# Optimization experiments

Hardware: AMD Instinct MI355X
Metric: run time of the kernel (lower is better)

The kernel has to match this reference:

```python
import jax, jax.numpy as jnp
import numpy as np

D_IN, H1, H2, B, K = 128, 128, 64, 262144, 4

def _mk(key, shape):
    return jax.random.normal(key, shape, dtype=jnp.float32) * 0.05

def setup_inputs() -> dict:
    key = jax.random.key(0)
    ks = jax.random.split(key, 40)
    inp = {
        'x': jax.random.normal(ks[0], (B, 96), dtype=jnp.float32),
        'u': jax.random.normal(ks[1], (B, 32), dtype=jnp.float32),
        'mix_factor': jax.random.uniform(ks[2], (1,), dtype=jnp.float32),
        'teacher_P': jax.random.uniform(ks[3], (K,), dtype=jnp.float32),
    }
    # main critic params (torch Linear: W [out,in], b [out])
    dims = [(H1, D_IN), (H1, H1), (H2, H1), (1, H2)] * 2  # l1..l4, l5..l8
    for i, (o, ii) in enumerate(dims):
        inp[f'W{i+1}'] = _mk(ks[4 + 2 * i], (o, ii))
        inp[f'b{i+1}'] = _mk(ks[5 + 2 * i], (o,))
    # stacked teacher params (K teachers), only l1,l2,l3,l5,l6,l7 are used
    tdims = {'1': (H1, D_IN), '2': (H1, H1), '3': (H2, H1), '5': (H1, D_IN), '6': (H1, H1), '7': (H2, H1)}
    j = 20
    for name, (o, ii) in tdims.items():
        inp[f'tW{name}'] = _mk(ks[j], (K, o, ii)); j += 1
        inp[f'tb{name}'] = _mk(ks[j], (K, o)); j += 1
    return inp

def reference(x, u, mix_factor, teacher_P, W1, b1, W2, b2, W3, b3, W4, b4, W5, b5, W6, b6, W7, b7, W8, b8, tW1, tb1, tW2, tb2, tW3, tb3, tW5, tb5, tW6, tb6, tW7, tb7):
    m = mix_factor  # [1], broadcasts
    P = teacher_P   # [K]
    xu = jnp.concatenate([x, u], axis=1)  # [B, 128]

    lin = lambda h, W, b: h @ W.T + b
    # teacher linear on shared input [B,I] -> [K,B,O]
    tlin0 = lambda h, W, b: jnp.einsum('bi,koi->kbo', h, W) + b[:, None, :]
    # teacher linear on per-teacher streams [K,B,I] -> [K,B,O]
    tlin = lambda h, W, b: jnp.einsum('kbi,koi->kbo', h, W) + b[:, None, :]
    mixsum = lambda ht: jnp.einsum('kbo,k->bo', ht, P)

    def head(W_a, b_a, W_b, b_b, W_c, b_c, W_d, b_d, tWa, tba, tWb, tbb, tWc, tbc):
        ht = tlin0(xu, tWa, tba)                                   # [K,B,128]
        h = jax.nn.relu(lin(xu, W_a, b_a) * (1 - m) + mixsum(ht) * m)
        ht = jax.nn.relu(ht)
        ht2 = tlin(ht, tWb, tbb)
        h = jax.nn.relu(lin(h, W_b, b_b) * (1 - m) + mixsum(ht2) * m)
        ht2 = jax.nn.relu(ht2)
        ht3 = tlin(ht2, tWc, tbc)
        h = jax.nn.relu(lin(h, W_c, b_c) * (1 - m) + mixsum(ht3) * m)
        return lin(h, W_d, b_d)                                    # [B,1]

    x1 = head(W1, b1, W2, b2, W3, b3, W4, b4, tW1, tb1, tW2, tb2, tW3, tb3)
    x2 = head(W5, b5, W6, b6, W7, b7, W8, b8, tW5, tb5, tW6, tb6, tW7, tb7)
    return (x1, x2)
```

## Files before the change

kernel.cpp:

```cpp
#include <hip/hip_runtime.h>
#include <hip/hip_bf16.h>
#include <stdint.h>

#define B_TOTAL 262144
#define TB 64
#define SLOT 16384
#define BUF1 81920
#define LDS_BYTES 163840
#define HEAD_W 204800

typedef short v8s __attribute__((ext_vector_type(8)));
typedef float v4f __attribute__((ext_vector_type(4)));

union Frag { uint4 q; uint32_t d[4]; v8s v; };

__device__ __forceinline__ unsigned short f2bf(float f) {
    uint32_t u = __float_as_uint(f);
    return (unsigned short)((u + 0x7FFFu + ((u >> 16) & 1u)) >> 16);
}
__device__ __forceinline__ uint32_t pack2(float a, float b) {
    union { __hip_bfloat162 h; uint32_t u; } p;
    p.h = __float22bfloat162_rn(make_float2(a, b));
    return p.u;
}


struct KParams {
    const float* x; const float* u; const float* mix; const float* P;
    const float* mb[6];
    const float* tb[6];
    const float* Wout[2];
    const float* bout[2];
    const unsigned short* wbf;
    float* out;
};

struct PrepParams { const float* src[12]; unsigned short* dst; };

__global__ __launch_bounds__(256) void prep_kernel(PrepParams pp) {
    const int ends[12] = {16384,81920,98304,163840,172032,204800,
                          221184,286720,303104,368640,376832,409600};
    int gi = (blockIdx.x * 256 + threadIdx.x) * 4;
    if (gi >= 409600) return;
    int s = 0;
    #pragma unroll
    for (int i = 0; i < 12; ++i) { if (gi >= ends[i]) s = i + 1; }
    int base = (s == 0) ? 0 : ends[s - 1];
    const float4 f = *(const float4*)(pp.src[s] + (gi - base));
    *(uint2*)(pp.dst + gi) = make_uint2(pack2(f.x, f.y), pack2(f.z, f.w));
}

__device__ __forceinline__ void stage_xu(char* lds, const float* x, const float* u,
                                         int rowBase, int tid)
{
    for (int G = tid; G < 1024; G += 256) {
        const int row = G >> 4;
        const int gg  = G & 15;
        const int grow = rowBase + row;
        float4 fa, fb;
        if (gg < 12) {
            const float* s2 = x + grow * 96 + gg * 8;
            fa = *(const float4*)s2; fb = *(const float4*)(s2 + 4);
        } else {
            const float* s2 = u + grow * 32 + (gg - 12) * 8;
            fa = *(const float4*)s2; fb = *(const float4*)(s2 + 4);
        }
        *(uint4*)(lds + row * 256 + ((gg ^ (row & 15)) << 4)) =
            make_uint4(pack2(fa.x, fa.y), pack2(fa.z, fa.w),
                       pack2(fb.x, fb.y), pack2(fb.z, fb.w));
    }
}

template<bool SHARED_IN, int N>
__device__ __forceinline__ void layer_fwd(char* lds, int inOff, int outOff,
        const unsigned short* W, const float* mbias, const float* tbias,
        float c0, const float* cP, int lane, int wave,
        const float* Wout, float* pgrid)
{
    constexpr int OT = N / 64;
    constexpr bool FINAL = (N == 64);
    const int l15  = lane & 15;
    const int quad = lane >> 4;
    const int cg   = wave;

    v4f acc[5][OT][4];
    #pragma unroll
    for (int s = 0; s < 5; ++s)
        #pragma unroll
        for (int ot = 0; ot < OT; ++ot)
            #pragma unroll
            for (int bt = 0; bt < 4; ++bt)
                acc[s][ot][bt] = (v4f){0.f, 0.f, 0.f, 0.f};

    #pragma unroll
    for (int ks = 0; ks < 4; ++ks) {
        Frag xS[4];
        if constexpr (SHARED_IN) {
            #pragma unroll
            for (int bt = 0; bt < 4; ++bt) {
                const int row = bt * 16 + l15;
                const int gg  = ks * 4 + quad;
                xS[bt].q = *(const uint4*)(lds + inOff + row * 256 + ((gg ^ (row & 15)) << 4));
            }
        }
        #pragma unroll
        for (int s = 0; s < 5; ++s) {
            Frag xF[4];
            if constexpr (!SHARED_IN) {
                #pragma unroll
                for (int bt = 0; bt < 4; ++bt) {
                    const int row = bt * 16 + l15;
                    const int gg  = ks * 4 + quad;
                    xF[bt].q = *(const uint4*)(lds + inOff + s * SLOT + row * 256
                                               + ((gg ^ (row & 15)) << 4));
                }
            }
            Frag wF[OT];
            #pragma unroll
            for (int ot = 0; ot < OT; ++ot) {
                const int o = cg * (OT * 16) + ot * 16 + l15;
                wF[ot].q = *(const uint4*)(W + s * (N * 128) + o * 128 + ks * 32 + quad * 8);
            }
            #pragma unroll
            for (int ot = 0; ot < OT; ++ot)
                #pragma unroll
                for (int bt = 0; bt < 4; ++bt)
                    acc[s][ot][bt] = __builtin_amdgcn_mfma_f32_16x16x32_bf16(
                        wF[ot].v, (SHARED_IN ? xS[bt].v : xF[bt].v), acc[s][ot][bt], 0, 0, 0);
        }
    }

    if constexpr (!FINAL) {
        #pragma unroll
        for (int ot = 0; ot < OT; ++ot) {
            const int obase = cg * 32 + ot * 16 + quad * 4;
            const float4 mB = *(const float4*)(mbias + obase);
            float4 tB[4];
            #pragma unroll
            for (int s = 0; s < 4; ++s)
                tB[s] = *(const float4*)(tbias + s * N + obase);
            #pragma unroll
            for (int bt = 0; bt < 4; ++bt) {
                const int row = bt * 16 + l15;
                char* ab = lds + outOff + row * 256 + (((obase >> 3) ^ (row & 15)) << 4)
                           + ((obase & 7) << 1);
                float vr[4];
                vr[0] = c0 * (acc[0][ot][bt][0] + mB.x);
                vr[1] = c0 * (acc[0][ot][bt][1] + mB.y);
                vr[2] = c0 * (acc[0][ot][bt][2] + mB.z);
                vr[3] = c0 * (acc[0][ot][bt][3] + mB.w);
                uint2 tw[4];
                #pragma unroll
                for (int s = 0; s < 4; ++s) {
                    float t0 = acc[s + 1][ot][bt][0] + tB[s].x;
                    float t1 = acc[s + 1][ot][bt][1] + tB[s].y;
                    float t2 = acc[s + 1][ot][bt][2] + tB[s].z;
                    float t3 = acc[s + 1][ot][bt][3] + tB[s].w;
                    vr[0] = fmaf(cP[s], t0, vr[0]);
                    vr[1] = fmaf(cP[s], t1, vr[1]);
                    vr[2] = fmaf(cP[s], t2, vr[2]);
                    vr[3] = fmaf(cP[s], t3, vr[3]);
                    tw[s] = make_uint2(pack2(fmaxf(t0, 0.f), fmaxf(t1, 0.f)),
                                       pack2(fmaxf(t2, 0.f), fmaxf(t3, 0.f)));
                }
                *(uint2*)ab = make_uint2(pack2(fmaxf(vr[0], 0.f), fmaxf(vr[1], 0.f)),
                                         pack2(fmaxf(vr[2], 0.f), fmaxf(vr[3], 0.f)));
                #pragma unroll
                for (int s = 0; s < 4; ++s)
                    *(uint2*)(ab + (s + 1) * SLOT) = tw[s];
            }
        }
    } else {
        const int obase = cg * 16 + quad * 4;
        const float4 mB = *(const float4*)(mbias + obase);
        float4 tB[4];
        #pragma unroll
        for (int s = 0; s < 4; ++s)
            tB[s] = *(const float4*)(tbias + s * N + obase);
        const float4 wo = *(const float4*)(Wout + obase);
        float psum[4];
        #pragma unroll
        for (int bt = 0; bt < 4; ++bt) {
            float vr[4];
            vr[0] = c0 * (acc[0][0][bt][0] + mB.x);
            vr[1] = c0 * (acc[0][0][bt][1] + mB.y);
            vr[2] = c0 * (acc[0][0][bt][2] + mB.z);
            vr[3] = c0 * (acc[0][0][bt][3] + mB.w);
            #pragma unroll
            for (int s = 0; s < 4; ++s) {
                vr[0] = fmaf(cP[s], acc[s + 1][0][bt][0] + tB[s].x, vr[0]);
                vr[1] = fmaf(cP[s], acc[s + 1][0][bt][1] + tB[s].y, vr[1]);
                vr[2] = fmaf(cP[s], acc[s + 1][0][bt][2] + tB[s].z, vr[2]);
                vr[3] = fmaf(cP[s], acc[s + 1][0][bt][3] + tB[s].w, vr[3]);
            }
            float pp = fmaxf(vr[0], 0.f) * wo.x + fmaxf(vr[1], 0.f) * wo.y
                     + fmaxf(vr[2], 0.f) * wo.z + fmaxf(vr[3], 0.f) * wo.w;
            pp += __shfl_xor(pp, 16);
            pp += __shfl_xor(pp, 32);
            psum[bt] = pp;
        }
        if (lane < 16) {
            #pragma unroll
            for (int bt = 0; bt < 4; ++bt)
                pgrid[cg * 64 + bt * 16 + lane] = psum[bt];
        }
    }
}

extern "C" __global__ __launch_bounds__(256, 1)
void critic_kernel(KParams p)
{
    extern __shared__ char lds[];
    const int tid  = threadIdx.x;
    const int lane = tid & 63;
    const int wave = tid >> 6;
    const int rowBase = blockIdx.x * TB;

    const float m  = p.mix[0];
    const float c0 = 1.f - m;
    float cP[4];
    #pragma unroll
    for (int k = 0; k < 4; ++k) cP[k] = m * p.P[k];

    stage_xu(lds, p.x, p.u, rowBase, tid);

    #pragma unroll 1
    for (int head = 0; head < 2; ++head) {
        __syncthreads();
        const unsigned short* wb = p.wbf + head * HEAD_W;
        const int hb = head * 3;

        layer_fwd<true, 128>(lds, 0, BUF1, wb, p.mb[hb + 0], p.tb[hb + 0],
                             c0, cP, lane, wave, nullptr, nullptr);
        __syncthreads();
        layer_fwd<false, 128>(lds, BUF1, 0, wb + 81920, p.mb[hb + 1], p.tb[hb + 1],
                              c0, cP, lane, wave, nullptr, nullptr);
        __syncthreads();
        layer_fwd<false, 64>(lds, 0, 0, wb + 163840, p.mb[hb + 2], p.tb[hb + 2],
                             c0, cP, lane, wave, p.Wout[head], (float*)(lds + BUF1));
        __syncthreads();

        if (tid < 64) {
            const float* pg = (const float*)(lds + BUF1);
            p.out[head * B_TOTAL + rowBase + tid] =
                p.bout[head][0] + pg[tid] + pg[64 + tid] + pg[128 + tid] + pg[192 + tid];
        }
        if (head == 0)
            stage_xu(lds, p.x, p.u, rowBase, tid);
    }
}

extern "C" void kernel_launch(void* const* d_in, const int* in_sizes, int n_in,
                              void* d_out, int out_size, void* d_ws, size_t ws_size,
                              hipStream_t stream)
{
    (void)in_sizes; (void)n_in; (void)out_size; (void)ws_size;

    PrepParams pp;
    const int sidx[12] = {4, 20, 6, 22, 8, 24, 12, 26, 14, 28, 16, 30};
    for (int i = 0; i < 12; ++i) pp.src[i] = (const float*)d_in[sidx[i]];
    pp.dst = (unsigned short*)d_ws;

    KParams kp;
    kp.x = (const float*)d_in[0];  kp.u = (const float*)d_in[1];
    kp.mix = (const float*)d_in[2]; kp.P = (const float*)d_in[3];
    const int mbi[6] = {5, 7, 9, 13, 15, 17};
    const int tbi[6] = {21, 23, 25, 27, 29, 31};
    for (int i = 0; i < 6; ++i) {
        kp.mb[i] = (const float*)d_in[mbi[i]];
        kp.tb[i] = (const float*)d_in[tbi[i]];
    }
    kp.Wout[0] = (const float*)d_in[10]; kp.Wout[1] = (const float*)d_in[18];
    kp.bout[0] = (const float*)d_in[11]; kp.bout[1] = (const float*)d_in[19];
    kp.wbf = (const unsigned short*)d_ws;
    kp.out = (float*)d_out;

    (void)hipFuncSetAttribute((const void*)critic_kernel,
                              hipFuncAttributeMaxDynamicSharedMemorySize, LDS_BYTES);

    hipLaunchKernelGGL(prep_kernel, dim3(400), dim3(256), 0, stream, pp);
    hipLaunchKernelGGL(critic_kernel, dim3(4096), dim3(256), LDS_BYTES, stream, kp);
}
```

Before: 882.2 us.

## Split layer work across eight waves with 16-column tiles per wave

The critic kernel goes from 256 to 512 threads per block. Each wave now computes one 16-column output tile instead of two, and the final 64-wide layer is split across wave pairs by batch tile. Launch bounds become (512,2) and the input staging loop stride is updated to match. The goal is more waves per CU to hide MFMA and LDS latency. In exchange, each activation fragment is reused across only one weight tile, so LDS reads double, and registers per thread are capped more tightly.

```diff
diff --git a/kernel.cpp b/kernel.cpp
--- a/kernel.cpp
+++ b/kernel.cpp
@@ -14,10 +14,6 @@
 
 union Frag { uint4 q; uint32_t d[4]; v8s v; };
 
-__device__ __forceinline__ unsigned short f2bf(float f) {
-    uint32_t u = __float_as_uint(f);
-    return (unsigned short)((u + 0x7FFFu + ((u >> 16) & 1u)) >> 16);
-}
 __device__ __forceinline__ uint32_t pack2(float a, float b) {
     union { __hip_bfloat162 h; uint32_t u; } p;
     p.h = __float22bfloat162_rn(make_float2(a, b));
@@ -53,7 +49,7 @@
 __device__ __forceinline__ void stage_xu(char* lds, const float* x, const float* u,
                                          int rowBase, int tid)
 {
-    for (int G = tid; G < 1024; G += 256) {
+    for (int G = tid; G < 1024; G += 512) {
         const int row = G >> 4;
         const int gg  = G & 15;
         const int grow = rowBase + row;
@@ -77,137 +73,123 @@
         float c0, const float* cP, int lane, int wave,
         const float* Wout, float* pgrid)
 {
-    constexpr int OT = N / 64;
     constexpr bool FINAL = (N == 64);
+    constexpr int NBT = FINAL ? 2 : 4;
     const int l15  = lane & 15;
     const int quad = lane >> 4;
-    const int cg   = wave;
-
-    v4f acc[5][OT][4];
+    const int colBase = FINAL ? ((wave >> 1) << 4) : (wave << 4);
+    const int btBase  = FINAL ? ((wave & 1) << 1) : 0;
+
+    v4f acc[5][NBT];
     #pragma unroll
     for (int s = 0; s < 5; ++s)
         #pragma unroll
-        for (int ot = 0; ot < OT; ++ot)
-            #pragma unroll
-            for (int bt = 0; bt < 4; ++bt)
-                acc[s][ot][bt] = (v4f){0.f, 0.f, 0.f, 0.f};
+        for (int bt = 0; bt < NBT; ++bt)
+            acc[s][bt] = (v4f){0.f, 0.f, 0.f, 0.f};
+
+    const unsigned short* wRow = W + (colBase + l15) * 128 + quad * 8;
 
     #pragma unroll
     for (int ks = 0; ks < 4; ++ks) {
-        Frag xS[4];
+        Frag xS[NBT];
+        const int gg = ks * 4 + quad;
         if constexpr (SHARED_IN) {
             #pragma unroll
-            for (int bt = 0; bt < 4; ++bt) {
-                const int row = bt * 16 + l15;
-                const int gg  = ks * 4 + quad;
+            for (int bt = 0; bt < NBT; ++bt) {
+                const int row = (btBase + bt) * 16 + l15;
                 xS[bt].q = *(const uint4*)(lds + inOff + row * 256 + ((gg ^ (row & 15)) << 4));
             }
         }
         #pragma unroll
         for (int s = 0; s < 5; ++s) {
-            Frag xF[4];
+            Frag xF[NBT];
             if constexpr (!SHARED_IN) {
                 #pragma unroll
-                for (int bt = 0; bt < 4; ++bt) {
-                    const int row = bt * 16 + l15;
-                    const int gg  = ks * 4 + quad;
+                for (int bt = 0; bt < NBT; ++bt) {
+                    const int row = (btBase + bt) * 16 + l15;
                     xF[bt].q = *(const uint4*)(lds + inOff + s * SLOT + row * 256
                                                + ((gg ^ (row & 15)) << 4));
                 }
             }
-            Frag wF[OT];
-            #pragma unroll
-            for (int ot = 0; ot < OT; ++ot) {
-                const int o = cg * (OT * 16) + ot * 16 + l15;
-                wF[ot].q = *(const uint4*)(W + s * (N * 128) + o * 128 + ks * 32 + quad * 8);
-            }
-            #pragma unroll
-            for (int ot = 0; ot < OT; ++ot)
-                #pragma unroll
-                for (int bt = 0; bt < 4; ++bt)
-                    acc[s][ot][bt] = __builtin_amdgcn_mfma_f32_16x16x32_bf16(
-                        wF[ot].v, (SHARED_IN ? xS[bt].v : xF[bt].v), acc[s][ot][bt], 0, 0, 0);
-        }
-    }
+            Frag wF;
+            wF.q = *(const uint4*)(wRow + s * (N * 128) + ks * 32);
+            #pragma unroll
+            for (int bt = 0; bt < NBT; ++bt)
+                acc[s][bt] = __builtin_amdgcn_mfma_f32_16x16x32_bf16(
+                    wF.v, (SHARED_IN ? xS[bt].v : xF[bt].v), acc[s][bt], 0, 0, 0);
+        }
+    }
+
+    const int obase = colBase + quad * 4;
+    const float4 mB = *(const float4*)(mbias + obase);
+    float4 tB[4];
+    #pragma unroll
+    for (int s = 0; s < 4; ++s)
+        tB[s] = *(const float4*)(tbias + s * N + obase);
 
     if constexpr (!FINAL) {
         #pragma unroll
-        for (int ot = 0; ot < OT; ++ot) {
-            const int obase = cg * 32 + ot * 16 + quad * 4;
-            const float4 mB = *(const float4*)(mbias + obase);
-            float4 tB[4];
+        for (int bt = 0; bt < 4; ++bt) {
+            const int row = bt * 16 + l15;
+            char* ab = lds + outOff + row * 256 + (((obase >> 3) ^ (row & 15)) << 4)
+                       + ((obase & 7) << 1);
+            float vr[4];
+            vr[0] = c0 * (acc[0][bt][0] + mB.x);
+            vr[1] = c0 * (acc[0][bt][1] + mB.y);
+            vr[2] = c0 * (acc[0][bt][2] + mB.z);
+            vr[3] = c0 * (acc[0][bt][3] + mB.w);
+            uint2 tw[4];
+            #pragma unroll
+            for (int s = 0; s < 4; ++s) {
+                float t0 = acc[s + 1][bt][0] + tB[s].x;
+                float t1 = acc[s + 1][bt][1] + tB[s].y;
+                float t2 = acc[s + 1][bt][2] + tB[s].z;
+                float t3 = acc[s + 1][bt][3] + tB[s].w;
+                vr[0] = fmaf(cP[s], t0, vr[0]);
+                vr[1] = fmaf(cP[s], t1, vr[1]);
+                vr[2] = fmaf(cP[s], t2, vr[2]);
+                vr[3] = fmaf(cP[s], t3, vr[3]);
+                tw[s] = make_uint2(pack2(fmaxf(t0, 0.f), fmaxf(t1, 0.f)),
+                                   pack2(fmaxf(t2, 0.f), fmaxf(t3, 0.f)));
+            }
+            *(uint2*)ab = make_uint2(pack2(fmaxf(vr[0], 0.f), fmaxf(vr[1], 0.f)),
+                                     pack2(fmaxf(vr[2], 0.f), fmaxf(vr[3], 0.f)));
             #pragma unroll
             for (int s = 0; s < 4; ++s)
-                tB[s] = *(const float4*)(tbias + s * N + obase);
-            #pragma unroll
-            for (int bt = 0; bt < 4; ++bt) {
-                const int row = bt * 16 + l15;
-                char* ab = lds + outOff + row * 256 + (((obase >> 3) ^ (row & 15)) << 4)
-                           + ((obase & 7) << 1);
-                float vr[4];
-                vr[0] = c0 * (acc[0][ot][bt][0] + mB.x);
-                vr[1] = c0 * (acc[0][ot][bt][1] + mB.y);
-                vr[2] = c0 * (acc[0][ot][bt][2] + mB.z);
-                vr[3] = c0 * (acc[0][ot][bt][3] + mB.w);
-                uint2 tw[4];
-                #pragma unroll
-                for (int s = 0; s < 4; ++s) {
-                    float t0 = acc[s + 1][ot][bt][0] + tB[s].x;
-                    float t1 = acc[s + 1][ot][bt][1] + tB[s].y;
-                    float t2 = acc[s + 1][ot][bt][2] + tB[s].z;
-                    float t3 = acc[s + 1][ot][bt][3] + tB[s].w;
-                    vr[0] = fmaf(cP[s], t0, vr[0]);
-                    vr[1] = fmaf(cP[s], t1, vr[1]);
-                    vr[2] = fmaf(cP[s], t2, vr[2]);
-                    vr[3] = fmaf(cP[s], t3, vr[3]);
-                    tw[s] = make_uint2(pack2(fmaxf(t0, 0.f), fmaxf(t1, 0.f)),
-                                       pack2(fmaxf(t2, 0.f), fmaxf(t3, 0.f)));
-                }
-                *(uint2*)ab = make_uint2(pack2(fmaxf(vr[0], 0.f), fmaxf(vr[1], 0.f)),
-                                         pack2(fmaxf(vr[2], 0.f), fmaxf(vr[3], 0.f)));
-                #pragma unroll
-                for (int s = 0; s < 4; ++s)
-                    *(uint2*)(ab + (s + 1) * SLOT) = tw[s];
-            }
+                *(uint2*)(ab + (s + 1) * SLOT) = tw[s];
         }
     } else {
-        const int obase = cg * 16 + quad * 4;
-        const float4 mB = *(const float4*)(mbias + obase);
-        float4 tB[4];
-        #pragma unroll
-        for (int s = 0; s < 4; ++s)
-            tB[s] = *(const float4*)(tbias + s * N + obase);
         const float4 wo = *(const float4*)(Wout + obase);
-        float psum[4];
-        #pragma unroll
-        for (int bt = 0; bt < 4; ++bt) {
+        float psum[NBT];
+        #pragma unroll
+        for (int j = 0; j < NBT; ++j) {
             float vr[4];
-            vr[0] = c0 * (acc[0][0][bt][0] + mB.x);
-            vr[1] = c0 * (acc[0][0][bt][1] + mB.y);
-            vr[2] = c0 * (acc[0][0][bt][2] + mB.z);
-            vr[3] = c0 * (acc[0][0][bt][3] + mB.w);
+            vr[0] = c0 * (acc[0][j][0] + mB.x);
+            vr[1] = c0 * (acc[0][j][1] + mB.y);
+            vr[2] = c0 * (acc[0][j][2] + mB.z);
+            vr[3] = c0 * (acc[0][j][3] + mB.w);
             #pragma unroll
             for (int s = 0; s < 4; ++s) {
-                vr[0] = fmaf(cP[s], acc[s + 1][0][bt][0] + tB[s].x, vr[0]);
-                vr[1] = fmaf(cP[s], acc[s + 1][0][bt][1] + tB[s].y, vr[1]);
-                vr[2] = fmaf(cP[s], acc[s + 1][0][bt][2] + tB[s].z, vr[2]);
-                vr[3] = fmaf(cP[s], acc[s + 1][0][bt][3] + tB[s].w, vr[3]);
+                vr[0] = fmaf(cP[s], acc[s + 1][j][0] + tB[s].x, vr[0]);
+                vr[1] = fmaf(cP[s], acc[s + 1][j][1] + tB[s].y, vr[1]);
+                vr[2] = fmaf(cP[s], acc[s + 1][j][2] + tB[s].z, vr[2]);
+                vr[3] = fmaf(cP[s], acc[s + 1][j][3] + tB[s].w, vr[3]);
             }
             float pp = fmaxf(vr[0], 0.f) * wo.x + fmaxf(vr[1], 0.f) * wo.y
                      + fmaxf(vr[2], 0.f) * wo.z + fmaxf(vr[3], 0.f) * wo.w;
             pp += __shfl_xor(pp, 16);
             pp += __shfl_xor(pp, 32);
-            psum[bt] = pp;
+            psum[j] = pp;
         }
         if (lane < 16) {
             #pragma unroll
-            for (int bt = 0; bt < 4; ++bt)
-                pgrid[cg * 64 + bt * 16 + lane] = psum[bt];
-        }
-    }
-}
-
-extern "C" __global__ __launch_bounds__(256, 1)
+            for (int j = 0; j < NBT; ++j)
+                pgrid[(wave >> 1) * 64 + (btBase + j) * 16 + lane] = psum[j];
+        }
+    }
+}
+
+extern "C" __global__ __launch_bounds__(512, 2)
 void critic_kernel(KParams p)
 {
     extern __shared__ char lds[];
@@ -279,5 +261,5 @@
                               hipFuncAttributeMaxDynamicSharedMemorySize, LDS_BYTES);
 
     hipLaunchKernelGGL(prep_kernel, dim3(400), dim3(256), 0, stream, pp);
-    hipLaunchKernelGGL(critic_kernel, dim3(4096), dim3(256), LDS_BYTES, stream, kp);
-}
+    hipLaunchKernelGGL(critic_kernel, dim3(4096), dim3(512), LDS_BYTES, stream, kp);
+}
```

New measurement: 883.2 us. About the same (+0.1%).
